# Optimization experiments

Hardware: AMD Instinct MI355X
Metric: run time of the kernel (lower is better)

## Reference

```python
import jax, jax.numpy as jnp
import numpy as np

B, H, M, DH = 8, 32, 8, 64  # batch, spatial h=w, heads, dim_head
C = M * DH
HW = H * H


def _make_pos_idx(h: int) -> np.ndarray:
    # A[i, j] = j - i, matching tf.constant([range(i, i+h) for i in range(0, -h, -1)])
    A = np.arange(h)[None, :] - np.arange(h)[:, None]
    horiz = np.tile(A, (h, h))                              # (h^2, h^2)
    vert = np.repeat(np.repeat(A, h, axis=0), h, axis=1)    # (h^2, h^2)
    return (2 * h - 1) * (vert + h - 1) + (horiz + h - 1)   # values in [0, (2h-1)^2)


def setup_inputs() -> dict:
    key = jax.random.key(0)
    ks = jax.random.split(key, 4)
    x = jax.random.normal(ks[0], (B, H, H, C), dtype=jnp.float32)
    w_qkv = jax.random.normal(ks[1], (DH, 3 * DH), dtype=jnp.float32) * (1.0 / np.sqrt(DH))
    b_qkv = jnp.zeros((3 * DH,), dtype=jnp.float32)
    w_ht = jax.random.normal(ks[2], (C, C), dtype=jnp.float32) * (1.0 / np.sqrt(C))
    b_ht = jnp.zeros((C,), dtype=jnp.float32)
    # Glorot-normal scalar table over (2h-1)^2 relative positions
    n_rel = (2 * H - 1) ** 2
    pos_table = jax.random.normal(ks[3], (n_rel,), dtype=jnp.float32) * np.float32(np.sqrt(2.0 / (n_rel + 1)))
    pos_idx = jnp.asarray(_make_pos_idx(H), dtype=jnp.int32)  # (HW, HW)
    return {"x": x, "w_qkv": w_qkv, "b_qkv": b_qkv, "w_ht": w_ht, "b_ht": b_ht,
            "pos_table": pos_table, "pos_idx": pos_idx}


def reference(x, w_qkv, b_qkv, w_ht, b_ht, pos_table, pos_idx):
    b, h, w, c = x.shape
    d_h = c // M
    # split heads into the batch dim: (b*M, h, w, d_h)
    xh = x.reshape(b, h, w, M, d_h).transpose(0, 3, 1, 2, 4).reshape(b * M, h, w, d_h)
    # 1x1 conv == per-pixel dense
    qkv = xh @ w_qkv + b_qkv                       # (b*M, h, w, 3*DH)
    qkv = qkv.reshape(b * M, h * w, DH, 3)
    q, k, v = qkv[..., 0], qkv[..., 1], qkv[..., 2]
    q = q / jnp.sqrt(jnp.float32(DH))
    att = jnp.einsum('bic,bjc->bij', q, k)         # (b*M, HW, HW)
    pos_emb = pos_table[pos_idx]                   # (HW, HW) gathered bias
    att = jax.nn.softmax(att + pos_emb, axis=-1)
    o = jnp.einsum('bij,bjc->bic', att, v)         # (b*M, HW, DH)
    o = o.reshape(b, M, h, w, d_h).transpose(0, 2, 3, 1, 4).reshape(b, h, w, c)
    out = o @ w_ht + b_ht                          # 1x1 head_transform conv
    return (out, att, pos_emb)
```

## Files before the change

kernel.cpp:

```cpp
#include <hip/hip_runtime.h>
#include <hip/hip_bf16.h>

typedef __attribute__((ext_vector_type(8))) __bf16 bf16x8;
typedef __attribute__((ext_vector_type(8))) short  s16x8;
typedef __attribute__((ext_vector_type(4))) short  s16x4;
typedef __attribute__((ext_vector_type(4))) float  f32x4;

#define HW2 1024
#define CDIM 512

static __device__ __forceinline__ unsigned short f2b(float f) {
  __hip_bfloat16 h = __float2bfloat16(f);
  return __builtin_bit_cast(unsigned short, h);
}

static __device__ __forceinline__ f32x4 mfma16(s16x8 a, s16x8 b, f32x4 c) {
  return __builtin_amdgcn_mfma_f32_16x16x32_bf16(
      __builtin_bit_cast(bf16x8, a), __builtin_bit_cast(bf16x8, b), c, 0, 0, 0);
}

static __device__ __forceinline__ void lds_fence() {
  asm volatile("s_waitcnt lgkmcnt(0)" ::: "memory");
  __builtin_amdgcn_sched_barrier(0);
}

__global__ __launch_bounds__(256) void k_prep(
    const float* __restrict__ w_qkv, const float* __restrict__ w_ht,
    const float* __restrict__ table, const int* __restrict__ idx,
    unsigned short* __restrict__ Wtq, unsigned short* __restrict__ Wtk,
    unsigned short* __restrict__ Wtv, unsigned short* __restrict__ WhtT,
    float* __restrict__ pe) {
  int blk = blockIdx.x;
  if (blk < 16) {
    int i = blk * 256 + threadIdx.x;
    int c = i >> 6, k = i & 63;
    const float* src = w_qkv + k * 192 + 3 * c;
    Wtq[i] = f2b(src[0] * 0.125f);
    Wtk[i] = f2b(src[1]);
    Wtv[i] = f2b(src[2]);
  } else if (blk < 1040) {
    int i = (blk - 16) * 256 + threadIdx.x;
    int c = i >> 9, k = i & 511;
    WhtT[i] = f2b(w_ht[k * 512 + c]);
  } else {
    int i = (blk - 1040) * 256 + threadIdx.x;
    #pragma unroll
    for (int j = 0; j < 4; ++j) {
      int p = i + j * 262144;
      pe[p] = table[idx[p]];
    }
  }
}

__global__ __launch_bounds__(256) void k_qkv(const float* __restrict__ x,
    const float* __restrict__ b_qkv,
    const unsigned short* __restrict__ Wtq, const unsigned short* __restrict__ Wtk,
    const unsigned short* __restrict__ Wtv,
    unsigned short* __restrict__ Qb, unsigned short* __restrict__ Kb,
    unsigned short* __restrict__ Vt) {
  int bm = blockIdx.x >> 4;
  int pt = blockIdx.x & 15;
  int wid = threadIdx.x >> 6, lane = threadIdx.x & 63;
  int l15 = lane & 15, lg = lane >> 4;
  int b = bm >> 3, m = bm & 7;
  int pbase = pt * 64 + wid * 16;

  int pA = pbase + l15;
  const float* xp = x + (size_t)(b * HW2 + pA) * CDIM + m * 64 + lg * 8;
  f32x4 xv0 = *(const f32x4*)(xp);
  f32x4 xv1 = *(const f32x4*)(xp + 4);
  f32x4 xv2 = *(const f32x4*)(xp + 32);
  f32x4 xv3 = *(const f32x4*)(xp + 36);
  s16x8 a0, a1;
  #pragma unroll
  for (int j = 0; j < 4; ++j) {
    a0[j]     = (short)f2b(xv0[j]);
    a0[4 + j] = (short)f2b(xv1[j]);
    a1[j]     = (short)f2b(xv2[j]);
    a1[4 + j] = (short)f2b(xv3[j]);
  }

  f32x4 acc[12];
  #pragma unroll
  for (int ct = 0; ct < 12; ++ct) acc[ct] = (f32x4){0.f, 0.f, 0.f, 0.f};

  #pragma unroll
  for (int ct = 0; ct < 12; ++ct) {
    const unsigned short* W = (ct < 4) ? Wtq : (ct < 8 ? Wtk : Wtv);
    int c = (ct & 3) * 16 + l15;
    const unsigned short* wp = W + c * 64 + lg * 8;
    s16x8 b0 = *(const s16x8*)(wp);
    s16x8 b1 = *(const s16x8*)(wp + 32);
    if (ct < 8) {
      acc[ct] = mfma16(b0, a0, acc[ct]);
      acc[ct] = mfma16(b1, a1, acc[ct]);
    } else {
      acc[ct] = mfma16(a0, b0, acc[ct]);
      acc[ct] = mfma16(a1, b1, acc[ct]);
    }
  }

  #pragma unroll
  for (int ct = 0; ct < 8; ++ct) {
    int s = ct >> 2;
    int c0 = (ct & 3) * 16 + lg * 4;
    unsigned short* D = (s == 0) ? Qb : Kb;
    s16x4 pk;
    #pragma unroll
    for (int i = 0; i < 4; ++i) {
      float bias = b_qkv[3 * (c0 + i) + s];
      if (s == 0) bias *= 0.125f;
      pk[i] = (short)f2b(acc[ct][i] + bias);
    }
    *(s16x4*)(D + (size_t)(bm * HW2 + pbase + l15) * 64 + c0) = pk;
  }
  #pragma unroll
  for (int ct = 8; ct < 12; ++ct) {
    int c = (ct & 3) * 16 + l15;
    float bias = b_qkv[3 * c + 2];
    s16x4 pk;
    #pragma unroll
    for (int i = 0; i < 4; ++i) pk[i] = (short)f2b(acc[ct][i] + bias);
    *(s16x4*)(Vt + ((size_t)bm * 64 + c) * HW2 + pbase + lg * 4) = pk;
  }
}

__global__ __launch_bounds__(256, 3) void k_attn(
    const unsigned short* __restrict__ Qb, const unsigned short* __restrict__ Kb,
    const unsigned short* __restrict__ Vt, const float* __restrict__ ptab,
    float* __restrict__ att, unsigned short* __restrict__ O) {
  int r8 = blockIdx.x & 7;
  int kk = blockIdx.x >> 3;
  int qt = kk & 63;
  int bm = ((kk >> 6) << 3) | r8;
  int wid = threadIdx.x >> 6, lane = threadIdx.x & 63;
  int l15 = lane & 15, lg = lane >> 4;

  __shared__ unsigned short P[16][1032];
  __shared__ __align__(16) float stg[4][16][64];
  __shared__ float redm[4][16];
  __shared__ float reds[4][16];

  const unsigned short* qp = Qb + (size_t)(bm * HW2 + qt * 16 + l15) * 64 + lg * 8;
  s16x8 qa0 = *(const s16x8*)qp;
  s16x8 qa1 = *(const s16x8*)(qp + 32);

  f32x4 acc[16];
  const unsigned short* kbase = Kb + (size_t)bm * HW2 * 64;
  #pragma unroll
  for (int ct = 0; ct < 16; ++ct) {
    int col = wid * 256 + ct * 16 + l15;
    const unsigned short* kp = kbase + (size_t)col * 64 + lg * 8;
    s16x8 kb0 = *(const s16x8*)kp;
    s16x8 kb1 = *(const s16x8*)(kp + 32);
    f32x4 a = (f32x4){0.f, 0.f, 0.f, 0.f};
    a = mfma16(kb0, qa0, a);
    a = mfma16(kb1, qa1, a);
    acc[ct] = a;
  }

  int cb = 1984 - 63 * (qt >> 1) - ((qt & 1) << 4) - l15;
  float pm = -1e30f;
  #pragma unroll
  for (int ct = 0; ct < 16; ++ct) {
    int c0 = wid * 256 + ct * 16 + lg * 4;
    int t0 = 63 * (c0 >> 5) + (c0 & 31) + cb;
    f32x4 pv;
    __builtin_memcpy(&pv, ptab + t0, 16);
    #pragma unroll
    for (int i = 0; i < 4; ++i) {
      float v = acc[ct][i] + pv[i];
      acc[ct][i] = v;
      pm = fmaxf(pm, v);
    }
  }
  pm = fmaxf(pm, __shfl_xor(pm, 16));
  pm = fmaxf(pm, __shfl_xor(pm, 32));
  if (lane < 16) redm[wid][l15] = pm;
  __syncthreads();
  float mrow = fmaxf(fmaxf(redm[0][l15], redm[1][l15]),
                     fmaxf(redm[2][l15], redm[3][l15]));

  float ps = 0.f;
  #pragma unroll
  for (int ct = 0; ct < 16; ++ct) {
    #pragma unroll
    for (int i = 0; i < 4; ++i) {
      float e = __expf(acc[ct][i] - mrow);
      acc[ct][i] = e;
      ps += e;
    }
  }
  ps += __shfl_xor(ps, 16);
  ps += __shfl_xor(ps, 32);
  if (lane < 16) reds[wid][l15] = ps;
  __syncthreads();
  float inv = 1.0f / (reds[0][l15] + reds[1][l15] + reds[2][l15] + reds[3][l15]);

  float* abase = att + (size_t)(bm * HW2 + qt * 16) * HW2 + wid * 256;
  #pragma unroll
  for (int q = 0; q < 4; ++q) {
    #pragma unroll
    for (int t4 = 0; t4 < 4; ++t4) {
      int ct = q * 4 + t4;
      int c0 = wid * 256 + ct * 16 + lg * 4;
      f32x4 vv;
      #pragma unroll
      for (int i = 0; i < 4; ++i) vv[i] = acc[ct][i] * inv;
      int cw = (t4 * 4 + lg) ^ (l15 & 7);
      *(f32x4*)&stg[wid][l15][cw * 4] = vv;
      s16x4 pk;
      #pragma unroll
      for (int i = 0; i < 4; ++i) pk[i] = (short)f2b(vv[i]);
      *(s16x4*)&P[l15][c0] = pk;
    }
    lds_fence();
    f32x4 vals[4];
    #pragma unroll
    for (int i = 0; i < 4; ++i) {
      int r = i * 4 + lg;
      int cr = l15 ^ (r & 7);
      vals[i] = *(const f32x4*)&stg[wid][r][cr * 4];
    }
    lds_fence();
    #pragma unroll
    for (int i = 0; i < 4; ++i) {
      int r = i * 4 + lg;
      *(f32x4*)(abase + (size_t)r * HW2 + q * 64 + l15 * 4) = vals[i];
    }
  }
  __syncthreads();

  f32x4 o = (f32x4){0.f, 0.f, 0.f, 0.f};
  const unsigned short* vbase = Vt + (size_t)(bm * 64 + wid * 16 + l15) * HW2;
  #pragma unroll
  for (int kt = 0; kt < 32; ++kt) {
    s16x8 vb = *(const s16x8*)(vbase + kt * 32 + lg * 8);
    s16x8 pa = *(const s16x8*)&P[l15][kt * 32 + lg * 8];
    o = mfma16(vb, pa, o);
  }
  s16x4 ok;
  #pragma unroll
  for (int i = 0; i < 4; ++i) ok[i] = (short)f2b(o[i]);
  *(s16x4*)(O + (size_t)(bm * HW2 + qt * 16 + l15) * 64 + wid * 16 + lg * 4) = ok;
}

__global__ __launch_bounds__(256) void k_ht(
    const unsigned short* __restrict__ O, const unsigned short* __restrict__ WhtT,
    const float* __restrict__ b_ht, float* __restrict__ out) {
  int rt = blockIdx.x >> 1;
  int ch = blockIdx.x & 1;
  int wid = threadIdx.x >> 6, lane = threadIdx.x & 63;
  int wr = wid >> 1, wc = wid & 1;
  int l15 = lane & 15, lg = lane >> 4;
  int b = (rt * 32) >> 10;
  int p0 = (rt * 32) & 1023;

  __shared__ unsigned short A[32][520];

  int t = threadIdx.x;
  #pragma unroll
  for (int j = 0; j < 8; ++j) {
    int idx = t * 8 + j * 2048;
    int row = idx >> 9;
    int k0 = idx & 511;
    int m = k0 >> 6, kk = k0 & 63;
    const unsigned short* src = O + (size_t)((b * 8 + m) * HW2 + p0 + row) * 64 + kk;
    *(s16x8*)&A[row][k0] = *(const s16x8*)src;
  }
  __syncthreads();

  f32x4 acc[8];
  #pragma unroll
  for (int ct = 0; ct < 8; ++ct) acc[ct] = (f32x4){0.f, 0.f, 0.f, 0.f};

  #pragma unroll
  for (int kt = 0; kt < 16; ++kt) {
    s16x8 a = *(const s16x8*)&A[wr * 16 + l15][kt * 32 + lg * 8];
    #pragma unroll
    for (int ct = 0; ct < 8; ++ct) {
      int col = ch * 256 + wc * 128 + ct * 16 + l15;
      s16x8 bf = *(const s16x8*)(WhtT + (size_t)col * 512 + kt * 32 + lg * 8);
      acc[ct] = mfma16(bf, a, acc[ct]);
    }
  }

  int rp = rt * 32 + wr * 16 + l15;
  #pragma unroll
  for (int ct = 0; ct < 8; ++ct) {
    int c0 = ch * 256 + wc * 128 + ct * 16 + lg * 4;
    f32x4 bb = *(const f32x4*)(b_ht + c0);
    f32x4 ov;
    #pragma unroll
    for (int i = 0; i < 4; ++i) ov[i] = acc[ct][i] + bb[i];
    *(f32x4*)(out + (size_t)rp * 512 + c0) = ov;
  }
}

extern "C" void kernel_launch(void* const* d_in, const int* in_sizes, int n_in,
                              void* d_out, int out_size, void* d_ws, size_t ws_size,
                              hipStream_t stream) {
  const float* x         = (const float*)d_in[0];
  const float* w_qkv     = (const float*)d_in[1];
  const float* b_qkv     = (const float*)d_in[2];
  const float* w_ht      = (const float*)d_in[3];
  const float* b_ht      = (const float*)d_in[4];
  const float* pos_table = (const float*)d_in[5];
  const int*   pos_idx   = (const int*)d_in[6];

  float* out = (float*)d_out;
  float* att = out + 4194304;
  float* pe  = att + 67108864;

  char* ws = (char*)d_ws;
  unsigned short* Qb   = (unsigned short*)(ws);
  unsigned short* Kb   = (unsigned short*)(ws + (8u  << 20));
  unsigned short* Vt   = (unsigned short*)(ws + (16u << 20));
  unsigned short* O    = (unsigned short*)(ws + (24u << 20));
  unsigned short* Wtq  = (unsigned short*)(ws + (32u << 20));
  unsigned short* Wtk  = Wtq + 4096;
  unsigned short* Wtv  = Wtk + 4096;
  unsigned short* WhtT = (unsigned short*)(ws + (32u << 20) + 65536);

  k_prep<<<2064, 256, 0, stream>>>(w_qkv, w_ht, pos_table, pos_idx,
                                   Wtq, Wtk, Wtv, WhtT, pe);
  k_qkv <<<1024, 256, 0, stream>>>(x, b_qkv, Wtq, Wtk, Wtv, Qb, Kb, Vt);
  k_attn<<<4096, 256, 0, stream>>>(Qb, Kb, Vt, pos_table, att, O);
  k_ht  <<<512,  256, 0, stream>>>(O, WhtT, b_ht, out);
}
```

Before: 207.5 us.

## Halve attention LDS footprint by staging P in two passes and raise occupancy

The attention kernel now keeps the bf16 probability fragments in registers and writes them to shared memory in two halves, reusing one buffer that also serves as the fp32 transpose staging area. This cuts LDS per block from about 49 KB to about 17 KB. The launch bound is raised from 3 to 6 blocks per SIMD to exploit the smaller footprint. In exchange it adds extra __syncthreads and 16 packed registers per thread, and the tighter register cap may cause spills.

```diff
diff --git a/kernel.cpp b/kernel.cpp
--- a/kernel.cpp
+++ b/kernel.cpp
@@ -125,7 +125,7 @@
   }
 }
 
-__global__ __launch_bounds__(256, 3) void k_attn(
+__global__ __launch_bounds__(256, 6) void k_attn(
     const unsigned short* __restrict__ Qb, const unsigned short* __restrict__ Kb,
     const unsigned short* __restrict__ Vt, const float* __restrict__ ptab,
     float* __restrict__ att, unsigned short* __restrict__ O) {
@@ -136,8 +136,7 @@
   int wid = threadIdx.x >> 6, lane = threadIdx.x & 63;
   int l15 = lane & 15, lg = lane >> 4;
 
-  __shared__ unsigned short P[16][1032];
-  __shared__ __align__(16) float stg[4][16][64];
+  __shared__ __align__(16) unsigned char buf[16 * 520 * 2];
   __shared__ float redm[4][16];
   __shared__ float reds[4][16];
 
@@ -197,22 +196,23 @@
   __syncthreads();
   float inv = 1.0f / (reds[0][l15] + reds[1][l15] + reds[2][l15] + reds[3][l15]);
 
+  float* stgw = (float*)buf + wid * 1024;
   float* abase = att + (size_t)(bm * HW2 + qt * 16) * HW2 + wid * 256;
+  s16x4 pkr[16];
   #pragma unroll
   for (int q = 0; q < 4; ++q) {
     #pragma unroll
     for (int t4 = 0; t4 < 4; ++t4) {
       int ct = q * 4 + t4;
-      int c0 = wid * 256 + ct * 16 + lg * 4;
       f32x4 vv;
       #pragma unroll
       for (int i = 0; i < 4; ++i) vv[i] = acc[ct][i] * inv;
       int cw = (t4 * 4 + lg) ^ (l15 & 7);
-      *(f32x4*)&stg[wid][l15][cw * 4] = vv;
+      *(f32x4*)&stgw[l15 * 64 + cw * 4] = vv;
       s16x4 pk;
       #pragma unroll
       for (int i = 0; i < 4; ++i) pk[i] = (short)f2b(vv[i]);
-      *(s16x4*)&P[l15][c0] = pk;
+      pkr[ct] = pk;
     }
     lds_fence();
     f32x4 vals[4];
@@ -220,7 +220,7 @@
     for (int i = 0; i < 4; ++i) {
       int r = i * 4 + lg;
       int cr = l15 ^ (r & 7);
-      vals[i] = *(const f32x4*)&stg[wid][r][cr * 4];
+      vals[i] = *(const f32x4*)&stgw[r * 64 + cr * 4];
     }
     lds_fence();
     #pragma unroll
@@ -231,14 +231,37 @@
   }
   __syncthreads();
 
+  unsigned short (*Ph)[520] = (unsigned short(*)[520])buf;
+  const unsigned short* vbase = Vt + (size_t)(bm * 64 + wid * 16 + l15) * HW2;
   f32x4 o = (f32x4){0.f, 0.f, 0.f, 0.f};
-  const unsigned short* vbase = Vt + (size_t)(bm * 64 + wid * 16 + l15) * HW2;
-  #pragma unroll
-  for (int kt = 0; kt < 32; ++kt) {
+
+  if (wid < 2) {
+    #pragma unroll
+    for (int ct = 0; ct < 16; ++ct)
+      *(s16x4*)&Ph[l15][wid * 256 + ct * 16 + lg * 4] = pkr[ct];
+  }
+  __syncthreads();
+  #pragma unroll
+  for (int kt = 0; kt < 16; ++kt) {
     s16x8 vb = *(const s16x8*)(vbase + kt * 32 + lg * 8);
-    s16x8 pa = *(const s16x8*)&P[l15][kt * 32 + lg * 8];
+    s16x8 pa = *(const s16x8*)&Ph[l15][kt * 32 + lg * 8];
     o = mfma16(vb, pa, o);
   }
+  __syncthreads();
+
+  if (wid >= 2) {
+    #pragma unroll
+    for (int ct = 0; ct < 16; ++ct)
+      *(s16x4*)&Ph[l15][(wid - 2) * 256 + ct * 16 + lg * 4] = pkr[ct];
+  }
+  __syncthreads();
+  #pragma unroll
+  for (int kt = 0; kt < 16; ++kt) {
+    s16x8 vb = *(const s16x8*)(vbase + 512 + kt * 32 + lg * 8);
+    s16x8 pa = *(const s16x8*)&Ph[l15][kt * 32 + lg * 8];
+    o = mfma16(vb, pa, o);
+  }
+
   s16x4 ok;
   #pragma unroll
   for (int i = 0; i < 4; ++i) ok[i] = (short)f2b(o[i]);
```

Result: slower. 242.3 us (+16.8%).
